# Optimization experiments

Measured on AMD Instinct MI355X. Metric: run time of the kernel, lower is better.

The kernel has to match this reference:

```python
import jax, jax.numpy as jnp
import numpy as np

S, B, NPG, NODE_DIM, EMB = 4, 64, 400, 7, 64
G = S * B            # graphs in batch = 256
N = G * NPG          # total nodes = 102400
EPG = 6400           # edges per graph (avg degree 16)
E = G * EPG          # 1,638,400 edges
NEG_SLOPE = 0.2


def setup_inputs() -> dict:
    key = jax.random.key(0)
    ks = jax.random.split(key, 16)
    rng = np.random.default_rng(0)
    base = np.repeat(np.arange(G, dtype=np.int64) * NPG, EPG)
    src = base + rng.integers(0, NPG, size=E)
    dst = base + rng.integers(0, NPG, size=E)
    edge_index = jnp.asarray(np.stack([src, dst]), dtype=jnp.int64)
    s0 = 1.0 / np.sqrt(NODE_DIM)
    s = 1.0 / np.sqrt(EMB)
    return {
        'x': jax.random.normal(ks[0], (N, NODE_DIM), jnp.float32),
        'edge_index': edge_index,
        'reachable': jax.random.randint(ks[1], (N,), 0, 2, jnp.int32),
        'Wl0': jax.random.normal(ks[2], (NODE_DIM, EMB), jnp.float32) * s0,
        'Wr0': jax.random.normal(ks[3], (NODE_DIM, EMB), jnp.float32) * s0,
        'bl0': jnp.zeros((EMB,), jnp.float32),
        'br0': jnp.zeros((EMB,), jnp.float32),
        'att0': jax.random.normal(ks[4], (EMB,), jnp.float32) * s,
        'bias0': jnp.zeros((EMB,), jnp.float32),
        'Wl': jax.random.normal(ks[5], (4, EMB, EMB), jnp.float32) * s,
        'Wr': jax.random.normal(ks[6], (4, EMB, EMB), jnp.float32) * s,
        'bl': jnp.zeros((4, EMB), jnp.float32),
        'br': jnp.zeros((4, EMB), jnp.float32),
        'att': jax.random.normal(ks[7], (4, EMB), jnp.float32) * s,
        'bias': jnp.zeros((4, EMB), jnp.float32),
    }


def _gatv2_layer(h, src, dst, Wl_, bl_, Wr_, br_, att_, bias_):
    # GATv2Conv, heads=1, concat=True, share_weights=False
    xl = h @ Wl_ + bl_                       # [N, C] source transform
    xr = h @ Wr_ + br_                       # [N, C] dest transform
    e = jax.nn.leaky_relu(xl[src] + xr[dst], NEG_SLOPE) @ att_   # [E]
    m = jax.ops.segment_max(e, dst, num_segments=N)
    ex = jnp.exp(e - m[dst])
    denom = jax.ops.segment_sum(ex, dst, num_segments=N)
    alpha = ex / denom[dst]                  # segment softmax over incoming edges
    out = jax.ops.segment_sum(alpha[:, None] * xl[src], dst, num_segments=N)
    return out + bias_


def reference(x, edge_index, reachable, Wl0, Wr0, bl0, br0, att0, bias0, Wl, Wr, bl, br, att, bias):
    # GATv2Conv default add_self_loops=True
    loops = jnp.arange(N, dtype=edge_index.dtype)
    src = jnp.concatenate([edge_index[0], loops])
    dst = jnp.concatenate([edge_index[1], loops])

    h = jax.nn.relu(_gatv2_layer(x, src, dst, Wl0, bl0, Wr0, br0, att0, bias0))
    for i in range(4):
        h = _gatv2_layer(h, src, dst, Wl[i], bl[i], Wr[i], br[i], att[i], bias[i])
        if i < 3:
            h = jax.nn.relu(h)  # no activation after the final (5th) layer

    # decoupled_batch = batch[:N//S] repeated S times (nodes are graph-contiguous)
    dec = jnp.tile(jnp.repeat(jnp.arange(B, dtype=jnp.float32), NPG), S)       # [N]
    # num_nodes list padded with zeros to N, sliced to N//S, repeated S times
    nn_full = jnp.concatenate([jnp.full((G,), NPG, jnp.float32), jnp.zeros((N - G,), jnp.float32)])
    num_nodes_col = jnp.tile(nn_full[: N // S], S)                              # [N]

    feats = jnp.concatenate(
        [h, dec[:, None], reachable.astype(jnp.float32)[:, None], num_nodes_col[:, None]], axis=1)
    return feats.reshape(S, N // S, EMB + 3)
```

## Files before the change

### kernel.cpp

```cpp
#include <hip/hip_runtime.h>


static constexpr int N_NODES = 102400;
static constexpr int N_GRAPH = 256;
static constexpr int NPG     = 400;
static constexpr int EPG     = 6400;
static constexpr int E_IN    = 1638400;
static constexpr int CSTR    = EPG + NPG;
static constexpr int E_TOT   = E_IN + N_NODES;
static constexpr int XSTR    = 68;
static constexpr int EBLK    = 1024;


__global__ __launch_bounds__(256)
void k_init(int* __restrict__ cursor, int* __restrict__ off) {
    int i = blockIdx.x * 256 + threadIdx.x;
    if (i < N_NODES) cursor[i] = 1;
    if (i == 0) off[N_NODES] = E_TOT;
}

__global__ __launch_bounds__(256)
void k_count(const int* __restrict__ ei, int* __restrict__ cursor) {
    int e = blockIdx.x * 256 + threadIdx.x;
    if (e >= E_IN) return;
    unsigned d = (unsigned)ei[E_IN + e];
    if (d < (unsigned)N_NODES) atomicAdd(&cursor[d], 1);
}

__global__ __launch_bounds__(512)
void k_scan(int* __restrict__ cursor, int* __restrict__ off,
            unsigned short* __restrict__ csr) {
    __shared__ int s[512];
    int g = blockIdx.x, t = threadIdx.x;
    int base = g * NPG;
    int cnt = (t < NPG) ? cursor[base + t] : 0;
    s[t] = cnt;
    for (int d = 1; d < 512; d <<= 1) {
        __syncthreads();
        int v = (t >= d) ? s[t - d] : 0;
        __syncthreads();
        s[t] += v;
    }
    __syncthreads();
    if (t < NPG) {
        int o = g * CSTR + (s[t] - cnt);
        off[base + t] = o;
        cursor[base + t] = o + 1;
        csr[o] = (unsigned short)t;
    }
}

__global__ __launch_bounds__(256)
void k_scatter(const int* __restrict__ ei, int* __restrict__ cursor,
               unsigned short* __restrict__ csr) {
    int e = blockIdx.x * 256 + threadIdx.x;
    if (e >= E_IN) return;
    unsigned s = (unsigned)ei[e];
    unsigned d = (unsigned)ei[E_IN + e];
    if (d >= (unsigned)N_NODES || s >= (unsigned)N_NODES) return;
    int pos = atomicAdd(&cursor[d], 1);
    csr[pos] = (unsigned short)(s % NPG);
}


#define FMA16(hk, wp) {                                                        \
    float4 w0_ = *(const float4*)&(wp)[0];                                     \
    float4 w1_ = *(const float4*)&(wp)[4];                                     \
    float4 w2_ = *(const float4*)&(wp)[8];                                     \
    float4 w3_ = *(const float4*)&(wp)[12];                                    \
    acc0  += (hk) * w0_.x; acc1  += (hk) * w0_.y;                              \
    acc2  += (hk) * w0_.z; acc3  += (hk) * w0_.w;                              \
    acc4  += (hk) * w1_.x; acc5  += (hk) * w1_.y;                              \
    acc6  += (hk) * w1_.z; acc7  += (hk) * w1_.w;                              \
    acc8  += (hk) * w2_.x; acc9  += (hk) * w2_.y;                              \
    acc10 += (hk) * w2_.z; acc11 += (hk) * w2_.w;                              \
    acc12 += (hk) * w3_.x; acc13 += (hk) * w3_.y;                              \
    acc14 += (hk) * w3_.z; acc15 += (hk) * w3_.w; }

template<int K>
__global__ __launch_bounds__(256)
void k_transform(const float* __restrict__ h, const float* __restrict__ Wl,
                 const float* __restrict__ Wr, const float* __restrict__ bl,
                 const float* __restrict__ br, float* __restrict__ xcat) {
    int bid  = blockIdx.x;
    int half = bid & 1;
    int tid  = threadIdx.x;
    int lane = tid & 63;
    int node = (bid >> 1) * 64 + lane;
    int c0   = __builtin_amdgcn_readfirstlane((tid >> 6) * 16);
    const float* __restrict__ W  = half ? Wr : Wl;
    const float* __restrict__ bb = half ? br : bl;

    float acc0 = 0.f, acc1 = 0.f, acc2 = 0.f, acc3 = 0.f;
    float acc4 = 0.f, acc5 = 0.f, acc6 = 0.f, acc7 = 0.f;
    float acc8 = 0.f, acc9 = 0.f, acc10 = 0.f, acc11 = 0.f;
    float acc12 = 0.f, acc13 = 0.f, acc14 = 0.f, acc15 = 0.f;

    constexpr int KQ = (K + 3) / 4;
    #pragma unroll
    for (int k4 = 0; k4 < KQ; ++k4) {
        float hv0, hv1, hv2, hv3;
        if constexpr ((K & 3) == 0) {
            float4 h4 = *(const float4*)&h[(size_t)node * K + k4 * 4];
            hv0 = h4.x; hv1 = h4.y; hv2 = h4.z; hv3 = h4.w;
        } else {
            const float* hr = &h[(size_t)node * K + k4 * 4];
            hv0 = (k4 * 4 + 0 < K) ? hr[0] : 0.f;
            hv1 = (k4 * 4 + 1 < K) ? hr[1] : 0.f;
            hv2 = (k4 * 4 + 2 < K) ? hr[2] : 0.f;
            hv3 = (k4 * 4 + 3 < K) ? hr[3] : 0.f;
        }
        if (k4 * 4 + 0 < K) FMA16(hv0, &W[(size_t)(k4 * 4 + 0) * 64 + c0]);
        if (k4 * 4 + 1 < K) FMA16(hv1, &W[(size_t)(k4 * 4 + 1) * 64 + c0]);
        if (k4 * 4 + 2 < K) FMA16(hv2, &W[(size_t)(k4 * 4 + 2) * 64 + c0]);
        if (k4 * 4 + 3 < K) FMA16(hv3, &W[(size_t)(k4 * 4 + 3) * 64 + c0]);
    }

    size_t ob = (size_t)node * 128 + half * 64 + c0;
    float4 r0 = {acc0  + bb[c0 + 0],  acc1  + bb[c0 + 1],
                 acc2  + bb[c0 + 2],  acc3  + bb[c0 + 3]};
    float4 r1 = {acc4  + bb[c0 + 4],  acc5  + bb[c0 + 5],
                 acc6  + bb[c0 + 6],  acc7  + bb[c0 + 7]};
    float4 r2 = {acc8  + bb[c0 + 8],  acc9  + bb[c0 + 9],
                 acc10 + bb[c0 + 10], acc11 + bb[c0 + 11]};
    float4 r3 = {acc12 + bb[c0 + 12], acc13 + bb[c0 + 13],
                 acc14 + bb[c0 + 14], acc15 + bb[c0 + 15]};
    *(float4*)&xcat[ob + 0]  = r0;
    *(float4*)&xcat[ob + 4]  = r1;
    *(float4*)&xcat[ob + 8]  = r2;
    *(float4*)&xcat[ob + 12] = r3;
}


__device__ __forceinline__ float red8(float x) {
    x += __int_as_float(__builtin_amdgcn_update_dpp(
            0, __float_as_int(x), 0xB1, 0xF, 0xF, true));
    x += __int_as_float(__builtin_amdgcn_update_dpp(
            0, __float_as_int(x), 0x4E, 0xF, 0xF, true));
    x += __int_as_float(__builtin_amdgcn_update_dpp(
            0, __float_as_int(x), 0x141, 0xF, 0xF, true));
    return x;
}

__device__ __forceinline__ float pe_of(const float* __restrict__ xl_s, int sl,
                                       int oc, float4 xra, float4 xrb,
                                       float4 ata, float4 atb,
                                       float4& va, float4& vb) {
    va = *(const float4*)&xl_s[sl * XSTR + oc * 8];
    vb = *(const float4*)&xl_s[sl * XSTR + oc * 8 + 4];
    float t, d;
    t = va.x + xra.x; d  = fmaxf(t, 0.2f * t) * ata.x;
    t = va.y + xra.y; d += fmaxf(t, 0.2f * t) * ata.y;
    t = va.z + xra.z; d += fmaxf(t, 0.2f * t) * ata.z;
    t = va.w + xra.w; d += fmaxf(t, 0.2f * t) * ata.w;
    t = vb.x + xrb.x; d += fmaxf(t, 0.2f * t) * atb.x;
    t = vb.y + xrb.y; d += fmaxf(t, 0.2f * t) * atb.y;
    t = vb.z + xrb.z; d += fmaxf(t, 0.2f * t) * atb.z;
    t = vb.w + xrb.w; d += fmaxf(t, 0.2f * t) * atb.w;
    return red8(d);
}

template<int RELU, int FINAL>
__global__ __launch_bounds__(EBLK)
void k_edge(const float* __restrict__ xcat, const unsigned short* __restrict__ csr,
            const int* __restrict__ off, const float* __restrict__ att,
            const float* __restrict__ bias, const int* __restrict__ reach,
            float* __restrict__ out) {
    __shared__ __align__(16) float xl_s[NPG * XSTR];
    __shared__ __align__(8) unsigned short csr_s[CSTR];
    __shared__ unsigned short off_s[404];
    int g = blockIdx.x;
    int gbase = g * NPG;
    int tid = threadIdx.x;

    for (int q = tid; q < NPG * 16; q += EBLK) {
        int node = q >> 4, c4 = q & 15;
        *(float4*)&xl_s[node * XSTR + c4 * 4] =
            *(const float4*)&xcat[(size_t)(gbase + node) * 128 + c4 * 4];
    }
    const unsigned int* csrg = (const unsigned int*)(csr + (size_t)g * CSTR);
    for (int q = tid; q < CSTR / 2; q += EBLK)
        ((unsigned int*)csr_s)[q] = csrg[q];
    for (int q = tid; q < NPG + 1; q += EBLK)
        off_s[q] = (unsigned short)(off[gbase + q] - g * CSTR);
    __syncthreads();

    int grp = tid >> 3;
    int oc  = tid & 7;
    float4 ata = *(const float4*)&att[oc * 8];
    float4 atb = *(const float4*)&att[oc * 8 + 4];
    float4 bia = *(const float4*)&bias[oc * 8];
    float4 bib = *(const float4*)&bias[oc * 8 + 4];

    for (int dl = grp; dl < NPG; dl += EBLK / 8) {
        int node = gbase + dl;
        float4 xra = *(const float4*)&xcat[(size_t)node * 128 + 64 + oc * 8];
        float4 xrb = *(const float4*)&xcat[(size_t)node * 128 + 64 + oc * 8 + 4];
        int beg = off_s[dl], end = off_s[dl + 1];

        float4 aa, ab, va, vb;
        float m = pe_of(xl_s, dl, oc, xra, xrb, ata, atb, va, vb);
        float dsum = 1.f;
        aa = va; ab = vb;

        int p = beg + 1;
        int pa = (p + 3) & ~3;
        if (pa > end) pa = end;
        for (; p < pa; ++p) {
            float4 wa, wb;
            float pe = pe_of(xl_s, csr_s[p], oc, xra, xrb, ata, atb, wa, wb);
            float cm = fmaxf(m, pe);
            float sc = __expf(m - cm);
            float ex = __expf(pe - cm);
            m = cm;
            dsum = dsum * sc + ex;
            aa.x = aa.x * sc + ex * wa.x;  aa.y = aa.y * sc + ex * wa.y;
            aa.z = aa.z * sc + ex * wa.z;  aa.w = aa.w * sc + ex * wa.w;
            ab.x = ab.x * sc + ex * wb.x;  ab.y = ab.y * sc + ex * wb.y;
            ab.z = ab.z * sc + ex * wb.z;  ab.w = ab.w * sc + ex * wb.w;
        }
        for (; p + 4 <= end; p += 4) {
            unsigned long long iv = *(const unsigned long long*)&csr_s[p];
            int s0 = (int)(iv & 0xFFFF),         s1 = (int)((iv >> 16) & 0xFFFF);
            int s2 = (int)((iv >> 32) & 0xFFFF), s3 = (int)(iv >> 48);
            float4 v0a, v0b, v1a, v1b, v2a, v2b, v3a, v3b;
            float p0 = pe_of(xl_s, s0, oc, xra, xrb, ata, atb, v0a, v0b);
            float p1 = pe_of(xl_s, s1, oc, xra, xrb, ata, atb, v1a, v1b);
            float p2 = pe_of(xl_s, s2, oc, xra, xrb, ata, atb, v2a, v2b);
            float p3 = pe_of(xl_s, s3, oc, xra, xrb, ata, atb, v3a, v3b);
            float cm = fmaxf(fmaxf(fmaxf(p0, p1), fmaxf(p2, p3)), m);
            float sc = __expf(m - cm);
            m = cm;
            float e0 = __expf(p0 - m), e1 = __expf(p1 - m);
            float e2 = __expf(p2 - m), e3 = __expf(p3 - m);
            dsum = dsum * sc + (e0 + e1) + (e2 + e3);
            aa.x = aa.x * sc + e0 * v0a.x + e1 * v1a.x + e2 * v2a.x + e3 * v3a.x;
            aa.y = aa.y * sc + e0 * v0a.y + e1 * v1a.y + e2 * v2a.y + e3 * v3a.y;
            aa.z = aa.z * sc + e0 * v0a.z + e1 * v1a.z + e2 * v2a.z + e3 * v3a.z;
            aa.w = aa.w * sc + e0 * v0a.w + e1 * v1a.w + e2 * v2a.w + e3 * v3a.w;
            ab.x = ab.x * sc + e0 * v0b.x + e1 * v1b.x + e2 * v2b.x + e3 * v3b.x;
            ab.y = ab.y * sc + e0 * v0b.y + e1 * v1b.y + e2 * v2b.y + e3 * v3b.y;
            ab.z = ab.z * sc + e0 * v0b.z + e1 * v1b.z + e2 * v2b.z + e3 * v3b.z;
            ab.w = ab.w * sc + e0 * v0b.w + e1 * v1b.w + e2 * v2b.w + e3 * v3b.w;
        }
        for (; p < end; ++p) {
            float4 wa, wb;
            float pe = pe_of(xl_s, csr_s[p], oc, xra, xrb, ata, atb, wa, wb);
            float cm = fmaxf(m, pe);
            float sc = __expf(m - cm);
            float ex = __expf(pe - cm);
            m = cm;
            dsum = dsum * sc + ex;
            aa.x = aa.x * sc + ex * wa.x;  aa.y = aa.y * sc + ex * wa.y;
            aa.z = aa.z * sc + ex * wa.z;  aa.w = aa.w * sc + ex * wa.w;
            ab.x = ab.x * sc + ex * wb.x;  ab.y = ab.y * sc + ex * wb.y;
            ab.z = ab.z * sc + ex * wb.z;  ab.w = ab.w * sc + ex * wb.w;
        }

        float inv = 1.0f / dsum;
        float4 ra = {aa.x * inv + bia.x, aa.y * inv + bia.y,
                     aa.z * inv + bia.z, aa.w * inv + bia.w};
        float4 rb = {ab.x * inv + bib.x, ab.y * inv + bib.y,
                     ab.z * inv + bib.z, ab.w * inv + bib.w};
        if (RELU) {
            ra.x = fmaxf(ra.x, 0.f); ra.y = fmaxf(ra.y, 0.f);
            ra.z = fmaxf(ra.z, 0.f); ra.w = fmaxf(ra.w, 0.f);
            rb.x = fmaxf(rb.x, 0.f); rb.y = fmaxf(rb.y, 0.f);
            rb.z = fmaxf(rb.z, 0.f); rb.w = fmaxf(rb.w, 0.f);
        }
        if (FINAL) {
            size_t b = (size_t)node * 67 + oc * 8;
            out[b + 0] = ra.x; out[b + 1] = ra.y;
            out[b + 2] = ra.z; out[b + 3] = ra.w;
            out[b + 4] = rb.x; out[b + 5] = rb.y;
            out[b + 6] = rb.z; out[b + 7] = rb.w;
        } else {
            *(float4*)&out[(size_t)node * 64 + oc * 8]     = ra;
            *(float4*)&out[(size_t)node * 64 + oc * 8 + 4] = rb;
        }
    }

    if (FINAL) {
        if (tid < NPG) {
            int node = gbase + tid;
            float dec = (float)(g & 63);
            float nn  = ((g & 63) == 0 && tid < 256) ? 400.f : 0.f;
            size_t b = (size_t)node * 67;
            out[b + 64] = dec;
            out[b + 65] = (float)reach[node];
            out[b + 66] = nn;
        }
    }
}


extern "C" void kernel_launch(void* const* d_in, const int* in_sizes, int n_in,
                              void* d_out, int out_size, void* d_ws, size_t ws_size,
                              hipStream_t stream) {
    const float* x     = (const float*)d_in[0];
    const int*   ei    = (const int*)d_in[1];
    const int*   reach = (const int*)d_in[2];
    const float* Wl0   = (const float*)d_in[3];
    const float* Wr0   = (const float*)d_in[4];
    const float* bl0   = (const float*)d_in[5];
    const float* br0   = (const float*)d_in[6];
    const float* att0  = (const float*)d_in[7];
    const float* bias0 = (const float*)d_in[8];
    const float* Wl    = (const float*)d_in[9];
    const float* Wr    = (const float*)d_in[10];
    const float* bl    = (const float*)d_in[11];
    const float* br    = (const float*)d_in[12];
    const float* att   = (const float*)d_in[13];
    const float* bias  = (const float*)d_in[14];
    float* out = (float*)d_out;

    char* ws = (char*)d_ws;
    float* h    = (float*)ws;  ws += (size_t)N_NODES * 64 * 4;
    float* xcat = (float*)ws;  ws += (size_t)N_NODES * 128 * 4;
    unsigned short* csr = (unsigned short*)ws;  ws += (size_t)E_TOT * 2;
    int* off    = (int*)ws;    ws += (size_t)(N_NODES + 1) * 4;
    int* cursor = (int*)ws;

    k_init   <<<(N_NODES + 255) / 256, 256, 0, stream>>>(cursor, off);
    k_count  <<<(E_IN + 255) / 256, 256, 0, stream>>>(ei, cursor);
    k_scan   <<<N_GRAPH, 512, 0, stream>>>(cursor, off, csr);
    k_scatter<<<(E_IN + 255) / 256, 256, 0, stream>>>(ei, cursor, csr);

    k_transform<7><<<N_NODES / 64 * 2, 256, 0, stream>>>(
        x, Wl0, Wr0, bl0, br0, xcat);
    k_edge<1, 0><<<N_GRAPH, EBLK, 0, stream>>>(xcat, csr, off, att0, bias0,
                                               reach, h);

    for (int i = 0; i < 4; ++i) {
        k_transform<64><<<N_NODES / 64 * 2, 256, 0, stream>>>(
            h, Wl + i * 4096, Wr + i * 4096, bl + i * 64, br + i * 64, xcat);
        if (i < 3) {
            k_edge<1, 0><<<N_GRAPH, EBLK, 0, stream>>>(
                xcat, csr, off, att + i * 64, bias + i * 64, reach, h);
        } else {
            k_edge<0, 1><<<N_GRAPH, EBLK, 0, stream>>>(
                xcat, csr, off, att + i * 64, bias + i * 64, reach, out);
        }
    }
}
```

Baseline: 559.7 us.

## Sort destination nodes by degree and use a single predicated 4-wide edge loop

The scan kernel now builds a per-graph counting sort of nodes by in-degree (capped at 63), and the edge kernel processes nodes in that order. Neighbouring 8-lane groups in a wavefront then hold nodes of similar degree, which reduces divergence. The scalar head and tail loops are replaced by one 4-wide loop that masks out-of-range slots with -1e30 logits. The launch bounds now also request 4 waves per SIMD. In exchange there is extra exp and LDS work on padded slots, plus the cost of building the order array.

```diff
diff --git a/kernel.cpp b/kernel.cpp
--- a/kernel.cpp
+++ b/kernel.cpp
@@ -29,12 +29,14 @@
 
 __global__ __launch_bounds__(512)
 void k_scan(int* __restrict__ cursor, int* __restrict__ off,
-            unsigned short* __restrict__ csr) {
+            unsigned short* __restrict__ csr, unsigned short* __restrict__ order) {
     __shared__ int s[512];
+    __shared__ int hist[64];
     int g = blockIdx.x, t = threadIdx.x;
     int base = g * NPG;
     int cnt = (t < NPG) ? cursor[base + t] : 0;
     s[t] = cnt;
+    if (t < 64) hist[t] = 0;
     for (int d = 1; d < 512; d <<= 1) {
         __syncthreads();
         int v = (t >= d) ? s[t - d] : 0;
@@ -42,11 +44,23 @@
         s[t] += v;
     }
     __syncthreads();
+    int deg = cnt < 63 ? cnt : 63;
+    if (t < NPG) atomicAdd(&hist[deg], 1);
     if (t < NPG) {
         int o = g * CSTR + (s[t] - cnt);
         off[base + t] = o;
         cursor[base + t] = o + 1;
         csr[o] = (unsigned short)t;
+    }
+    __syncthreads();
+    if (t == 0) {
+        int acc = 0;
+        for (int i = 0; i < 64; ++i) { int v = hist[i]; hist[i] = acc; acc += v; }
+    }
+    __syncthreads();
+    if (t < NPG) {
+        int pos = atomicAdd(&hist[deg], 1);
+        order[base + pos] = (unsigned short)t;
     }
 }
 
@@ -161,14 +175,15 @@
 }
 
 template<int RELU, int FINAL>
-__global__ __launch_bounds__(EBLK)
+__global__ __launch_bounds__(EBLK, 4)
 void k_edge(const float* __restrict__ xcat, const unsigned short* __restrict__ csr,
-            const int* __restrict__ off, const float* __restrict__ att,
-            const float* __restrict__ bias, const int* __restrict__ reach,
-            float* __restrict__ out) {
+            const int* __restrict__ off, const unsigned short* __restrict__ order,
+            const float* __restrict__ att, const float* __restrict__ bias,
+            const int* __restrict__ reach, float* __restrict__ out) {
     __shared__ __align__(16) float xl_s[NPG * XSTR];
     __shared__ __align__(8) unsigned short csr_s[CSTR];
     __shared__ unsigned short off_s[404];
+    __shared__ unsigned short ord_s[400];
     int g = blockIdx.x;
     int gbase = g * NPG;
     int tid = threadIdx.x;
@@ -183,6 +198,8 @@
         ((unsigned int*)csr_s)[q] = csrg[q];
     for (int q = tid; q < NPG + 1; q += EBLK)
         off_s[q] = (unsigned short)(off[gbase + q] - g * CSTR);
+    for (int q = tid; q < NPG; q += EBLK)
+        ord_s[q] = order[gbase + q];
     __syncthreads();
 
     int grp = tid >> 3;
@@ -192,7 +209,8 @@
     float4 bia = *(const float4*)&bias[oc * 8];
     float4 bib = *(const float4*)&bias[oc * 8 + 4];
 
-    for (int dl = grp; dl < NPG; dl += EBLK / 8) {
+    for (int ii = grp; ii < NPG; ii += EBLK / 8) {
+        int dl = ord_s[ii];
         int node = gbase + dl;
         float4 xra = *(const float4*)&xcat[(size_t)node * 128 + 64 + oc * 8];
         float4 xrb = *(const float4*)&xcat[(size_t)node * 128 + 64 + oc * 8 + 4];
@@ -203,36 +221,26 @@
         float dsum = 1.f;
         aa = va; ab = vb;
 
-        int p = beg + 1;
-        int pa = (p + 3) & ~3;
-        if (pa > end) pa = end;
-        for (; p < pa; ++p) {
-            float4 wa, wb;
-            float pe = pe_of(xl_s, csr_s[p], oc, xra, xrb, ata, atb, wa, wb);
-            float cm = fmaxf(m, pe);
-            float sc = __expf(m - cm);
-            float ex = __expf(pe - cm);
-            m = cm;
-            dsum = dsum * sc + ex;
-            aa.x = aa.x * sc + ex * wa.x;  aa.y = aa.y * sc + ex * wa.y;
-            aa.z = aa.z * sc + ex * wa.z;  aa.w = aa.w * sc + ex * wa.w;
-            ab.x = ab.x * sc + ex * wb.x;  ab.y = ab.y * sc + ex * wb.y;
-            ab.z = ab.z * sc + ex * wb.z;  ab.w = ab.w * sc + ex * wb.w;
-        }
-        for (; p + 4 <= end; p += 4) {
-            unsigned long long iv = *(const unsigned long long*)&csr_s[p];
-            int s0 = (int)(iv & 0xFFFF),         s1 = (int)((iv >> 16) & 0xFFFF);
-            int s2 = (int)((iv >> 32) & 0xFFFF), s3 = (int)(iv >> 48);
+        for (int p = beg + 1; p < end; p += 4) {
+            bool k1 = p + 1 < end, k2 = p + 2 < end, k3 = p + 3 < end;
+            int p1 = k1 ? p + 1 : end - 1;
+            int p2 = k2 ? p + 2 : end - 1;
+            int p3 = k3 ? p + 3 : end - 1;
+            int s0 = csr_s[p],  s1 = csr_s[p1];
+            int s2 = csr_s[p2], s3 = csr_s[p3];
             float4 v0a, v0b, v1a, v1b, v2a, v2b, v3a, v3b;
-            float p0 = pe_of(xl_s, s0, oc, xra, xrb, ata, atb, v0a, v0b);
-            float p1 = pe_of(xl_s, s1, oc, xra, xrb, ata, atb, v1a, v1b);
-            float p2 = pe_of(xl_s, s2, oc, xra, xrb, ata, atb, v2a, v2b);
-            float p3 = pe_of(xl_s, s3, oc, xra, xrb, ata, atb, v3a, v3b);
-            float cm = fmaxf(fmaxf(fmaxf(p0, p1), fmaxf(p2, p3)), m);
+            float q0 = pe_of(xl_s, s0, oc, xra, xrb, ata, atb, v0a, v0b);
+            float q1 = pe_of(xl_s, s1, oc, xra, xrb, ata, atb, v1a, v1b);
+            float q2 = pe_of(xl_s, s2, oc, xra, xrb, ata, atb, v2a, v2b);
+            float q3 = pe_of(xl_s, s3, oc, xra, xrb, ata, atb, v3a, v3b);
+            q1 = k1 ? q1 : -1e30f;
+            q2 = k2 ? q2 : -1e30f;
+            q3 = k3 ? q3 : -1e30f;
+            float cm = fmaxf(fmaxf(fmaxf(q0, q1), fmaxf(q2, q3)), m);
             float sc = __expf(m - cm);
             m = cm;
-            float e0 = __expf(p0 - m), e1 = __expf(p1 - m);
-            float e2 = __expf(p2 - m), e3 = __expf(p3 - m);
+            float e0 = __expf(q0 - m), e1 = __expf(q1 - m);
+            float e2 = __expf(q2 - m), e3 = __expf(q3 - m);
             dsum = dsum * sc + (e0 + e1) + (e2 + e3);
             aa.x = aa.x * sc + e0 * v0a.x + e1 * v1a.x + e2 * v2a.x + e3 * v3a.x;
             aa.y = aa.y * sc + e0 * v0a.y + e1 * v1a.y + e2 * v2a.y + e3 * v3a.y;
@@ -242,19 +250,6 @@
             ab.y = ab.y * sc + e0 * v0b.y + e1 * v1b.y + e2 * v2b.y + e3 * v3b.y;
             ab.z = ab.z * sc + e0 * v0b.z + e1 * v1b.z + e2 * v2b.z + e3 * v3b.z;
             ab.w = ab.w * sc + e0 * v0b.w + e1 * v1b.w + e2 * v2b.w + e3 * v3b.w;
-        }
-        for (; p < end; ++p) {
-            float4 wa, wb;
-            float pe = pe_of(xl_s, csr_s[p], oc, xra, xrb, ata, atb, wa, wb);
-            float cm = fmaxf(m, pe);
-            float sc = __expf(m - cm);
-            float ex = __expf(pe - cm);
-            m = cm;
-            dsum = dsum * sc + ex;
-            aa.x = aa.x * sc + ex * wa.x;  aa.y = aa.y * sc + ex * wa.y;
-            aa.z = aa.z * sc + ex * wa.z;  aa.w = aa.w * sc + ex * wa.w;
-            ab.x = ab.x * sc + ex * wb.x;  ab.y = ab.y * sc + ex * wb.y;
-            ab.z = ab.z * sc + ex * wb.z;  ab.w = ab.w * sc + ex * wb.w;
         }
 
         float inv = 1.0f / dsum;
@@ -319,27 +314,28 @@
     float* xcat = (float*)ws;  ws += (size_t)N_NODES * 128 * 4;
     unsigned short* csr = (unsigned short*)ws;  ws += (size_t)E_TOT * 2;
     int* off    = (int*)ws;    ws += (size_t)(N_NODES + 1) * 4;
-    int* cursor = (int*)ws;
+    int* cursor = (int*)ws;    ws += (size_t)N_NODES * 4;
+    unsigned short* order = (unsigned short*)ws;
 
     k_init   <<<(N_NODES + 255) / 256, 256, 0, stream>>>(cursor, off);
     k_count  <<<(E_IN + 255) / 256, 256, 0, stream>>>(ei, cursor);
-    k_scan   <<<N_GRAPH, 512, 0, stream>>>(cursor, off, csr);
+    k_scan   <<<N_GRAPH, 512, 0, stream>>>(cursor, off, csr, order);
     k_scatter<<<(E_IN + 255) / 256, 256, 0, stream>>>(ei, cursor, csr);
 
     k_transform<7><<<N_NODES / 64 * 2, 256, 0, stream>>>(
         x, Wl0, Wr0, bl0, br0, xcat);
-    k_edge<1, 0><<<N_GRAPH, EBLK, 0, stream>>>(xcat, csr, off, att0, bias0,
-                                               reach, h);
+    k_edge<1, 0><<<N_GRAPH, EBLK, 0, stream>>>(xcat, csr, off, order,
+                                               att0, bias0, reach, h);
 
     for (int i = 0; i < 4; ++i) {
         k_transform<64><<<N_NODES / 64 * 2, 256, 0, stream>>>(
             h, Wl + i * 4096, Wr + i * 4096, bl + i * 64, br + i * 64, xcat);
         if (i < 3) {
             k_edge<1, 0><<<N_GRAPH, EBLK, 0, stream>>>(
-                xcat, csr, off, att + i * 64, bias + i * 64, reach, h);
+                xcat, csr, off, order, att + i * 64, bias + i * 64, reach, h);
         } else {
             k_edge<0, 1><<<N_GRAPH, EBLK, 0, stream>>>(
-                xcat, csr, off, att + i * 64, bias + i * 64, reach, out);
-        }
-    }
-}
+                xcat, csr, off, order, att + i * 64, bias + i * 64, reach, out);
+        }
+    }
+}
```

Result: faster. 511.8 us (-8.5%).
